# Kernel tuning notes

Hardware: AMD Instinct MI355X
Metric: run time of the kernel (lower is better)

Reference implementation:

```python
import jax, jax.numpy as jnp
import numpy as np

DT = 0.05
T_STEPS = 100  # arange(0, 5, 0.05)


def setup_inputs() -> dict:
    key = jax.random.key(0)
    k1, k2, k3 = jax.random.split(key, 3)
    batch, dim = 256, 64
    initial_position = jax.random.normal(k1, (batch, dim), dtype=jnp.float32)
    # scale W down so dynamics stay bounded over the integration horizon
    W = jax.random.normal(k2, (dim, dim), dtype=jnp.float32) / jnp.sqrt(dim).astype(jnp.float32)
    b = jax.random.normal(k3, (dim,), dtype=jnp.float32) * 0.1
    return {"initial_position": initial_position, "W": W, "b": b}


def reference(initial_position, W, b):
    dim = W.shape[0]
    I = jnp.eye(dim, dtype=initial_position.dtype)
    expm_b = jax.vmap(jax.scipy.linalg.expm)  # batched matrix exponential

    def step(x, _):
        # x: (B, D). Regime mask from pre-activation z = x @ W^T + b.
        z = x @ W.T + b
        m = (z > 0).astype(x.dtype)                    # (B, D)
        W_eff = m[:, :, None] * W[None, :, :]          # rows of W scaled by mask
        b_eff = m * b                                  # (B, D)
        A = W_eff - I                                  # (B, D, D)
        A_exp = expm_b(A * DT)                         # (B, D, D)
        A_inv = jnp.linalg.pinv(A)                     # (B, D, D)
        Ainv_b = jnp.einsum('bij,bj->bi', A_inv, b_eff)
        B_term = jnp.einsum('bij,bj->bi', A_exp - I, Ainv_b)
        x_next = jnp.einsum('bij,bj->bi', A_exp, x) + B_term
        return x_next, x  # trajectory stores state BEFORE the update

    _, traj = jax.lax.scan(step, initial_position, None, length=T_STEPS)
    # traj: (T, B, D) -> (B, T, D)
    return jnp.transpose(traj, (1, 0, 2))
```

## Files before the change

### kernel.cpp

```cpp
#include <hip/hip_runtime.h>


#define DT_F 0.05f
#define T_STEPS 100
#define DD 64
#define KT 3
#define BATCH_MAX 256

__device__ __forceinline__ float matvec64(const float (&Wr)[DD], float w) {
    const int wi = __float_as_int(w);
    float a0 = 0.f, a1 = 0.f, a2 = 0.f, a3 = 0.f;
#pragma unroll
    for (int j = 0; j < DD; j += 4) {
        const float s0 = __int_as_float(__builtin_amdgcn_readlane(wi, j + 0));
        const float s1 = __int_as_float(__builtin_amdgcn_readlane(wi, j + 1));
        const float s2 = __int_as_float(__builtin_amdgcn_readlane(wi, j + 2));
        const float s3 = __int_as_float(__builtin_amdgcn_readlane(wi, j + 3));
        a0 = fmaf(Wr[j + 0], s0, a0);
        a1 = fmaf(Wr[j + 1], s1, a1);
        a2 = fmaf(Wr[j + 2], s2, a2);
        a3 = fmaf(Wr[j + 3], s3, a3);
    }
    return (a0 + a1) + (a2 + a3);
}

__global__ __launch_bounds__(64, 1)
void abla_kernel(const float* __restrict__ x0,
                 const float* __restrict__ W,
                 const float* __restrict__ bvec,
                 float* __restrict__ out) {
    const int batch = blockIdx.x;
    const int lane = threadIdx.x;

    float Wr[DD];
#pragma unroll
    for (int j = 0; j < DD; j += 4) {
        const float4 w4 = *reinterpret_cast<const float4*>(W + lane * DD + j);
        Wr[j + 0] = w4.x; Wr[j + 1] = w4.y; Wr[j + 2] = w4.z; Wr[j + 3] = w4.w;
    }
    const float bi = bvec[lane];
    float x = x0[batch * DD + lane];
    float* outp = out + (size_t)batch * T_STEPS * DD + lane;

    for (int t = 0; t < T_STEPS; ++t) {
        outp[(size_t)t * DD] = x;

        const float z = matvec64(Wr, x) + bi;
        const float m_dt = (z > 0.f) ? DT_F : 0.f;
        float w = m_dt * z - DT_F * x;
        float y = x + w;

#pragma unroll
        for (int k = 2; k <= KT; ++k) {
            const float v = matvec64(Wr, w);
            w = (m_dt * v - DT_F * w) * (1.0f / (float)k);
            y += w;
        }
        x = y;
    }
}

extern "C" void kernel_launch(void* const* d_in, const int* in_sizes, int n_in,
                              void* d_out, int out_size, void* d_ws, size_t ws_size,
                              hipStream_t stream) {
    const float* x0 = (const float*)d_in[0];
    const float* W  = (const float*)d_in[1];
    const float* b  = (const float*)d_in[2];
    float* out = (float*)d_out;

    int batch = in_sizes[0] / DD;
    if (batch <= 0 || batch > BATCH_MAX) batch = BATCH_MAX;
    abla_kernel<<<batch, DD, 0, stream>>>(x0, W, b, out);
}
```

Measured before the change: 118.0 us.

## Process two batch rows per wavefront to interleave independent matvec chains

Each block now integrates two batch trajectories at once, sharing the register-resident W rows and interleaving the two readlane/FMA chains for more instruction-level parallelism. The grid shrinks to half the blocks. This aims to hide the latency of the serial dependency chain, but it leaves half the CUs idle and doubles the per-wave instruction count. An odd batch size would read and write out of bounds.

```diff
diff --git a/kernel.cpp b/kernel.cpp
--- a/kernel.cpp
+++ b/kernel.cpp
@@ -7,21 +7,34 @@
 #define KT 3
 #define BATCH_MAX 256
 
-__device__ __forceinline__ float matvec64(const float (&Wr)[DD], float w) {
-    const int wi = __float_as_int(w);
+__device__ __forceinline__ void matvec2(const float (&Wr)[DD],
+                                        const float wA, const float wB,
+                                        float& rA, float& rB) {
+    const int ia = __float_as_int(wA);
+    const int ib = __float_as_int(wB);
     float a0 = 0.f, a1 = 0.f, a2 = 0.f, a3 = 0.f;
+    float c0 = 0.f, c1 = 0.f, c2 = 0.f, c3 = 0.f;
 #pragma unroll
     for (int j = 0; j < DD; j += 4) {
-        const float s0 = __int_as_float(__builtin_amdgcn_readlane(wi, j + 0));
-        const float s1 = __int_as_float(__builtin_amdgcn_readlane(wi, j + 1));
-        const float s2 = __int_as_float(__builtin_amdgcn_readlane(wi, j + 2));
-        const float s3 = __int_as_float(__builtin_amdgcn_readlane(wi, j + 3));
-        a0 = fmaf(Wr[j + 0], s0, a0);
-        a1 = fmaf(Wr[j + 1], s1, a1);
-        a2 = fmaf(Wr[j + 2], s2, a2);
-        a3 = fmaf(Wr[j + 3], s3, a3);
+        const float sa0 = __int_as_float(__builtin_amdgcn_readlane(ia, j + 0));
+        const float sa1 = __int_as_float(__builtin_amdgcn_readlane(ia, j + 1));
+        const float sa2 = __int_as_float(__builtin_amdgcn_readlane(ia, j + 2));
+        const float sa3 = __int_as_float(__builtin_amdgcn_readlane(ia, j + 3));
+        const float sb0 = __int_as_float(__builtin_amdgcn_readlane(ib, j + 0));
+        const float sb1 = __int_as_float(__builtin_amdgcn_readlane(ib, j + 1));
+        const float sb2 = __int_as_float(__builtin_amdgcn_readlane(ib, j + 2));
+        const float sb3 = __int_as_float(__builtin_amdgcn_readlane(ib, j + 3));
+        a0 = fmaf(Wr[j + 0], sa0, a0);
+        c0 = fmaf(Wr[j + 0], sb0, c0);
+        a1 = fmaf(Wr[j + 1], sa1, a1);
+        c1 = fmaf(Wr[j + 1], sb1, c1);
+        a2 = fmaf(Wr[j + 2], sa2, a2);
+        c2 = fmaf(Wr[j + 2], sb2, c2);
+        a3 = fmaf(Wr[j + 3], sa3, a3);
+        c3 = fmaf(Wr[j + 3], sb3, c3);
     }
-    return (a0 + a1) + (a2 + a3);
+    rA = (a0 + a1) + (a2 + a3);
+    rB = (c0 + c1) + (c2 + c3);
 }
 
 __global__ __launch_bounds__(64, 1)
@@ -29,7 +42,8 @@
                  const float* __restrict__ W,
                  const float* __restrict__ bvec,
                  float* __restrict__ out) {
-    const int batch = blockIdx.x;
+    const int bA = blockIdx.x * 2;
+    const int bB = bA + 1;
     const int lane = threadIdx.x;
 
     float Wr[DD];
@@ -39,24 +53,39 @@
         Wr[j + 0] = w4.x; Wr[j + 1] = w4.y; Wr[j + 2] = w4.z; Wr[j + 3] = w4.w;
     }
     const float bi = bvec[lane];
-    float x = x0[batch * DD + lane];
-    float* outp = out + (size_t)batch * T_STEPS * DD + lane;
+    float xA = x0[bA * DD + lane];
+    float xB = x0[bB * DD + lane];
+    float* outA = out + (size_t)bA * T_STEPS * DD + lane;
+    float* outB = out + (size_t)bB * T_STEPS * DD + lane;
 
     for (int t = 0; t < T_STEPS; ++t) {
-        outp[(size_t)t * DD] = x;
+#pragma unroll
+        for (int j = 0; j < DD; ++j) asm volatile("" : "+v"(Wr[j]));
 
-        const float z = matvec64(Wr, x) + bi;
-        const float m_dt = (z > 0.f) ? DT_F : 0.f;
-        float w = m_dt * z - DT_F * x;
-        float y = x + w;
+        outA[(size_t)t * DD] = xA;
+        outB[(size_t)t * DD] = xB;
+
+        float zA, zB;
+        matvec2(Wr, xA, xB, zA, zB);
+        zA += bi; zB += bi;
+        const float mA = (zA > 0.f) ? DT_F : 0.f;
+        const float mB = (zB > 0.f) ? DT_F : 0.f;
+        float wA = mA * zA - DT_F * xA;
+        float wB = mB * zB - DT_F * xB;
+        float yA = xA + wA;
+        float yB = xB + wB;
 
 #pragma unroll
         for (int k = 2; k <= KT; ++k) {
-            const float v = matvec64(Wr, w);
-            w = (m_dt * v - DT_F * w) * (1.0f / (float)k);
-            y += w;
+            float vA, vB;
+            matvec2(Wr, wA, wB, vA, vB);
+            wA = (mA * vA - DT_F * wA) * (1.0f / (float)k);
+            wB = (mB * vB - DT_F * wB) * (1.0f / (float)k);
+            yA += wA;
+            yB += wB;
         }
-        x = y;
+        xA = yA;
+        xB = yB;
     }
 }
 
@@ -70,5 +99,6 @@
 
     int batch = in_sizes[0] / DD;
     if (batch <= 0 || batch > BATCH_MAX) batch = BATCH_MAX;
-    abla_kernel<<<batch, DD, 0, stream>>>(x0, W, b, out);
+    const int pairs = (batch + 1) / 2;
+    abla_kernel<<<pairs, DD, 0, stream>>>(x0, W, b, out);
 }
```

Result: slower. 181.4 us (+53.7%).
